# Kernel tuning notes

Hardware: AMD Instinct MI355X
Metric: run time of the kernel (lower is better)

Reference implementation:

```python
import jax, jax.numpy as jnp
import numpy as np

N_POINTS = 262144
SP_FEAT = 128
HIDDEN = 64
EMBED = 256
NUM_SP = 4096
NUM_SP2 = 256
PAD_LIMIT = 64
MASK_RATIO = 0.6


def setup_inputs() -> dict:
    key = jax.random.key(0)
    ks = jax.random.split(key, 6)
    x = jax.random.normal(ks[0], (N_POINTS, SP_FEAT), jnp.float32)
    # point -> superpoint ids, sorted; force every superpoint non-empty
    idx10 = jax.random.randint(ks[1], (N_POINTS,), 0, NUM_SP)
    idx10 = jnp.sort(idx10.at[:NUM_SP].set(jnp.arange(NUM_SP))).astype(jnp.int32)
    # superpoint -> higher superpoint, balanced (16 per group, < PAD_LIMIT), sorted
    idx21 = ((jnp.arange(NUM_SP) * NUM_SP2) // NUM_SP).astype(jnp.int32)
    # deterministic mask: exactly int(NUM_SP * MASK_RATIO) superpoints masked
    mask_num = int(NUM_SP * MASK_RATIO)
    perm = jax.random.permutation(ks[2], NUM_SP)
    is_masked = jnp.zeros((NUM_SP,), bool).at[perm[:mask_num]].set(True)
    W1 = jax.random.normal(ks[3], (SP_FEAT, HIDDEN), jnp.float32) / np.sqrt(SP_FEAT).astype(np.float32)
    b1 = jnp.zeros((HIDDEN,), jnp.float32)
    W2 = jax.random.normal(ks[4], (HIDDEN, EMBED), jnp.float32) / np.sqrt(HIDDEN).astype(np.float32)
    b2 = jnp.zeros((EMBED,), jnp.float32)
    return {
        "full_features": x,
        "full_super_indices_10": idx10,
        "full_super_indices_21": idx21,
        "is_masked": is_masked,
        "W1": W1, "b1": b1, "W2": W2, "b2": b2,
    }


def _pad_scatter(tokens, idx21, flag):
    # tokens: [NUM_SP, C]; idx21 sorted sp->sp2 ids; flag: [NUM_SP] bool.
    # rank of each flagged superpoint within its sp2 group (in sp order)
    f = flag.astype(jnp.int32)
    cum = jnp.cumsum(f)                                            # inclusive global cumsum
    per_group = jax.ops.segment_sum(f, idx21, num_segments=NUM_SP2)
    prefix = jnp.concatenate([jnp.zeros((1,), jnp.int32), jnp.cumsum(per_group)[:-1]])
    rank = cum - 1 - prefix[idx21]                                 # 0-based slot within group
    slot = jnp.where(flag, rank, PAD_LIMIT)                        # PAD_LIMIT -> dropped
    out = jnp.zeros((NUM_SP2, PAD_LIMIT, tokens.shape[-1]), tokens.dtype)
    return out.at[idx21, slot].set(tokens, mode="drop")


def reference(full_features, full_super_indices_10, full_super_indices_21,
              is_masked, W1, b1, W2, b2):
    # per-point 2-layer MLP (gather is implicit: MLP is pointwise), then segment max
    h = jax.nn.relu(full_features @ W1 + b1)                       # [N, HIDDEN]
    h = jax.nn.relu(h @ W2 + b2)                                   # [N, EMBED]
    tok = jax.ops.segment_max(h, full_super_indices_10, num_segments=NUM_SP)  # [NUM_SP, EMBED]
    remain_tokens = _pad_scatter(tok, full_super_indices_21, ~is_masked)      # [NUM_SP2, PAD, EMBED]
    mask_tokens = _pad_scatter(tok, full_super_indices_21, is_masked)         # [NUM_SP2, PAD, EMBED]
    return (remain_tokens, mask_tokens)
```

## Files before the change

### kernel.cpp

```cpp
#include <hip/hip_runtime.h>
#include <hip/hip_bf16.h>

#define N_POINTS 262144
#define SP_FEAT 128
#define HIDDEN 64
#define EMBED 256
#define NUM_SP 4096
#define NUM_SP2 256
#define PAD_LIMIT 64
#define SLOTS 4
#define OS_STRIDE 268

typedef __bf16 bf16x8 __attribute__((ext_vector_type(8)));
typedef float floatx4 __attribute__((ext_vector_type(4)));
using bf16 = __hip_bfloat16;

__global__ void prep_kernel(const float* __restrict__ W1, const float* __restrict__ W2,
                            const int* __restrict__ idx10,
                            bf16* __restrict__ W1t, bf16* __restrict__ W2t,
                            int* __restrict__ start) {
    int i = blockIdx.x * blockDim.x + threadIdx.x;
    if (i < HIDDEN * SP_FEAT) {
        int n = i >> 7, k = i & 127;
        W1t[i] = __float2bfloat16(W1[k * HIDDEN + n]);
    } else if (i < HIDDEN * SP_FEAT + EMBED * HIDDEN) {
        int j = i - HIDDEN * SP_FEAT;
        int n = j >> 6, k = j & 63;
        W2t[j] = __float2bfloat16(W2[k * EMBED + n]);
    } else if (i <= HIDDEN * SP_FEAT + EMBED * HIDDEN + NUM_SP) {
        int s = i - (HIDDEN * SP_FEAT + EMBED * HIDDEN);
        if (s == NUM_SP) { start[s] = N_POINTS; return; }
        int a = 0, b = N_POINTS;
        while (a < b) { int m = (a + b) >> 1; if (idx10[m] < s) a = m + 1; else b = m; }
        start[s] = a;
    }
}

__global__ __launch_bounds__(256) void rank_kernel(
    const int* __restrict__ idx21, const void* __restrict__ is_masked,
    int* __restrict__ invR, int* __restrict__ invM) {
    __shared__ int encS;
    const int tid = threadIdx.x;
    if (tid == 0) encS = 0;
    __syncthreads();
    const unsigned char* mb = (const unsigned char*)is_masked;
    const int* mi = (const int*)is_masked;
    int local = 0;
    for (int p = tid; p < NUM_SP; p += 256)
        if ((p & 3) && mb[p]) local = 1;
    if (local) atomicOr(&encS, 1);
    __syncthreads();
    const int e = encS;

    const int g = tid;
    int a = 0, b = NUM_SP;
    while (a < b) { int m = (a + b) >> 1; if (idx21[m] < g) a = m + 1; else b = m; }
    int lo = a;
    b = NUM_SP;
    while (a < b) { int m = (a + b) >> 1; if (idx21[m] < g + 1) a = m + 1; else b = m; }
    int hi = a;
    int nR = 0, nM = 0;
    for (int s = lo; s < hi; ++s) {
        int msk = e ? (int)mb[s] : mi[s];
        if (msk) { if (nM < PAD_LIMIT) invM[g * PAD_LIMIT + nM] = s; nM++; }
        else     { if (nR < PAD_LIMIT) invR[g * PAD_LIMIT + nR] = s; nR++; }
    }
    for (int r = nR; r < PAD_LIMIT; ++r) invR[g * PAD_LIMIT + r] = -1;
    for (int r = nM; r < PAD_LIMIT; ++r) invM[g * PAD_LIMIT + r] = -1;
}

__global__ __launch_bounds__(256) void mlp_segmax_kernel(
    const float* __restrict__ X, const int* __restrict__ idx10,
    const int* __restrict__ start,
    const bf16* __restrict__ W1t, const float* __restrict__ b1,
    const bf16* __restrict__ W2t, const float* __restrict__ b2,
    float* __restrict__ partial)
{
    __shared__ __align__(16) char smemU[64 * OS_STRIDE * 2];
    __shared__ __align__(16) bf16 H1s[64][72];
    __shared__ int sIdx[64];
    bf16 (*Xs)[136]      = (bf16(*)[136])smemU;
    bf16 (*Os)[OS_STRIDE] = (bf16(*)[OS_STRIDE])smemU;

    const int tid  = threadIdx.x;
    const int lane = tid & 63;
    const int w    = tid >> 6;
    const int l15  = lane & 15;
    const int quad = lane >> 4;
    const int b    = blockIdx.x;
    const int m0   = b * 64;

    bf16x8 bw1[4];
    {
        const bf16* p = W1t + (16 * w + l15) * SP_FEAT + quad * 8;
#pragma unroll
        for (int ks = 0; ks < 4; ++ks) bw1[ks] = *(const bf16x8*)(p + 32 * ks);
    }
    bf16x8 bf2[4][2];
#pragma unroll
    for (int tn = 0; tn < 4; ++tn) {
        const bf16* p = W2t + (64 * w + 16 * tn + l15) * HIDDEN + quad * 8;
#pragma unroll
        for (int ks = 0; ks < 2; ++ks) bf2[tn][ks] = *(const bf16x8*)(p + 32 * ks);
    }
    float b2f[4];
#pragma unroll
    for (int tn = 0; tn < 4; ++tn) b2f[tn] = b2[64 * w + 16 * tn + l15];
    const float b1v = b1[16 * w + l15];

#pragma unroll
    for (int i = 0; i < 4; ++i) {
        int c   = tid + 256 * i;
        int row = c >> 4;
        int cc  = (c & 15) * 8;
        const float* src = X + (size_t)(m0 + row) * SP_FEAT + cc;
        float4 u0 = *(const float4*)src;
        float4 u1 = *(const float4*)(src + 4);
        union { bf16x8 v; bf16 h[8]; } u;
        u.h[0] = __float2bfloat16(u0.x); u.h[1] = __float2bfloat16(u0.y);
        u.h[2] = __float2bfloat16(u0.z); u.h[3] = __float2bfloat16(u0.w);
        u.h[4] = __float2bfloat16(u1.x); u.h[5] = __float2bfloat16(u1.y);
        u.h[6] = __float2bfloat16(u1.z); u.h[7] = __float2bfloat16(u1.w);
        *(bf16x8*)(&Xs[row][cc]) = u.v;
    }
    if (tid < 64) sIdx[tid] = idx10[m0 + tid];
    __syncthreads();

    floatx4 zero4 = {0.f, 0.f, 0.f, 0.f};
    floatx4 acc1[4] = {zero4, zero4, zero4, zero4};
#pragma unroll
    for (int ks = 0; ks < 4; ++ks) {
        int k = ks * 32 + quad * 8;
#pragma unroll
        for (int tm = 0; tm < 4; ++tm) {
            bf16x8 a = *(bf16x8*)(&Xs[16 * tm + l15][k]);
            acc1[tm] = __builtin_amdgcn_mfma_f32_16x16x32_bf16(a, bw1[ks], acc1[tm], 0, 0, 0);
        }
    }
#pragma unroll
    for (int tm = 0; tm < 4; ++tm) {
#pragma unroll
        for (int r = 0; r < 4; ++r) {
            float v = acc1[tm][r] + b1v;
            v = v > 0.f ? v : 0.f;
            H1s[16 * tm + quad * 4 + r][16 * w + l15] = __float2bfloat16(v);
        }
    }
    __syncthreads();

#pragma unroll
    for (int tm = 0; tm < 4; ++tm) {
        bf16x8 a0 = *(bf16x8*)(&H1s[16 * tm + l15][quad * 8]);
        bf16x8 a1 = *(bf16x8*)(&H1s[16 * tm + l15][32 + quad * 8]);
#pragma unroll
        for (int tn = 0; tn < 4; ++tn) {
            floatx4 acc = zero4;
            acc = __builtin_amdgcn_mfma_f32_16x16x32_bf16(a0, bf2[tn][0], acc, 0, 0, 0);
            acc = __builtin_amdgcn_mfma_f32_16x16x32_bf16(a1, bf2[tn][1], acc, 0, 0, 0);
#pragma unroll
            for (int r = 0; r < 4; ++r) {
                float v = acc[r] + b2f[tn];
                v = v > 0.f ? v : 0.f;
                Os[16 * tm + quad * 4 + r][64 * w + 16 * tn + l15] = __float2bfloat16(v);
            }
        }
    }
    __syncthreads();

    {
        int cur_sp = sIdx[0];
        float cur  = __bfloat162float(Os[0][tid]);
        for (int r = 1; r < 64; ++r) {
            int sp = sIdx[r];
            float v = __bfloat162float(Os[r][tid]);
            if (sp != cur_sp) {
                int slot = b - (start[cur_sp] >> 6);
                int* dst = (int*)(partial + ((size_t)cur_sp * SLOTS + (slot < 3 ? slot : 3)) * EMBED + tid);
                if (slot < 3) *(float*)dst = cur;
                else atomicMax(dst, __float_as_int(cur));
                cur_sp = sp;
                cur = v;
            } else {
                cur = fmaxf(cur, v);
            }
        }
        int slot = b - (start[cur_sp] >> 6);
        int* dst = (int*)(partial + ((size_t)cur_sp * SLOTS + (slot < 3 ? slot : 3)) * EMBED + tid);
        if (slot < 3) *(float*)dst = cur;
        else atomicMax(dst, __float_as_int(cur));
    }
}

__global__ __launch_bounds__(256) void scatter_kernel(
    const float* __restrict__ partial, const int* __restrict__ invR,
    const int* __restrict__ invM, float* __restrict__ out)
{
    const int bb   = blockIdx.x;
    const int g    = bb & (NUM_SP2 - 1);
    const int slab = bb >> 8;
    const int tid  = threadIdx.x;
    const int* tab = slab ? invM : invR;
    float* o = out + ((size_t)slab * NUM_SP2 + g) * PAD_LIMIT * EMBED;
#pragma unroll 4
    for (int row = 0; row < PAD_LIMIT; ++row) {
        int sp = tab[g * PAD_LIMIT + row];
        float v = 0.f;
        if (sp >= 0) {
            const float* p = partial + (size_t)sp * SLOTS * EMBED + tid;
            v = fmaxf(fmaxf(p[0], p[EMBED]), fmaxf(p[2 * EMBED], p[3 * EMBED]));
        }
        o[row * EMBED + tid] = v;
    }
}

extern "C" void kernel_launch(void* const* d_in, const int* in_sizes, int n_in,
                              void* d_out, int out_size, void* d_ws, size_t ws_size,
                              hipStream_t stream) {
    (void)in_sizes; (void)n_in; (void)ws_size; (void)out_size;
    const float* X        = (const float*)d_in[0];
    const int* idx10      = (const int*)d_in[1];
    const int* idx21      = (const int*)d_in[2];
    const void* is_masked = (const void*)d_in[3];
    const float* W1       = (const float*)d_in[4];
    const float* b1       = (const float*)d_in[5];
    const float* W2       = (const float*)d_in[6];
    const float* b2       = (const float*)d_in[7];
    float* out            = (float*)d_out;

    char* ws      = (char*)d_ws;
    float* partial = (float*)ws;
    bf16* W1t     = (bf16*)(ws + (size_t)NUM_SP * SLOTS * EMBED * 4);
    bf16* W2t     = W1t + HIDDEN * SP_FEAT;
    int*  start   = (int*)((char*)(W2t + EMBED * HIDDEN));
    int*  invR    = start + (NUM_SP + 2);
    int*  invM    = invR + NUM_SP2 * PAD_LIMIT;

    hipMemsetAsync(partial, 0, (size_t)NUM_SP * SLOTS * EMBED * sizeof(float), stream);

    const int prep_n = HIDDEN * SP_FEAT + EMBED * HIDDEN + NUM_SP + 1;
    prep_kernel<<<(prep_n + 255) / 256, 256, 0, stream>>>(W1, W2, idx10, W1t, W2t, start);
    rank_kernel<<<1, 256, 0, stream>>>(idx21, is_masked, invR, invM);
    mlp_segmax_kernel<<<N_POINTS / 64, 256, 0, stream>>>(
        X, idx10, start, W1t, b1, W2t, b2, partial);
    scatter_kernel<<<NUM_SP2 * 2, 256, 0, stream>>>(partial, invR, invM, out);
}
```

Measured before the change: 272.5 us.

## Fuse memset, prep and rank kernels; alias H1 into shared buffer; vectorize scatter

Folds the memset of the partial buffer, the weight transpose/start search and the rank computation into one fused prep launch, removing two launches plus a memset. In the MLP kernel, H1 is aliased into the shared X/O buffer, padding strides change and launch bounds request four blocks per CU, which reduces LDS use to raise occupancy; an extra barrier is added so H1 fragments are loaded into registers before the output tile overwrites them. The scatter kernel now uses float4 loads and stores. These are several unrelated tweaks, and the extra register-held fragments may add pressure.

```diff
diff --git a/kernel.cpp b/kernel.cpp
--- a/kernel.cpp
+++ b/kernel.cpp
@@ -9,38 +9,52 @@
 #define NUM_SP2 256
 #define PAD_LIMIT 64
 #define SLOTS 4
-#define OS_STRIDE 268
+#define OS_STRIDE 260
+#define H1_STRIDE 76
 
 typedef __bf16 bf16x8 __attribute__((ext_vector_type(8)));
 typedef float floatx4 __attribute__((ext_vector_type(4)));
 using bf16 = __hip_bfloat16;
 
-__global__ void prep_kernel(const float* __restrict__ W1, const float* __restrict__ W2,
-                            const int* __restrict__ idx10,
-                            bf16* __restrict__ W1t, bf16* __restrict__ W2t,
-                            int* __restrict__ start) {
-    int i = blockIdx.x * blockDim.x + threadIdx.x;
-    if (i < HIDDEN * SP_FEAT) {
-        int n = i >> 7, k = i & 127;
-        W1t[i] = __float2bfloat16(W1[k * HIDDEN + n]);
-    } else if (i < HIDDEN * SP_FEAT + EMBED * HIDDEN) {
-        int j = i - HIDDEN * SP_FEAT;
-        int n = j >> 6, k = j & 63;
-        W2t[j] = __float2bfloat16(W2[k * EMBED + n]);
-    } else if (i <= HIDDEN * SP_FEAT + EMBED * HIDDEN + NUM_SP) {
-        int s = i - (HIDDEN * SP_FEAT + EMBED * HIDDEN);
-        if (s == NUM_SP) { start[s] = N_POINTS; return; }
-        int a = 0, b = N_POINTS;
-        while (a < b) { int m = (a + b) >> 1; if (idx10[m] < s) a = m + 1; else b = m; }
-        start[s] = a;
-    }
-}
-
-__global__ __launch_bounds__(256) void rank_kernel(
-    const int* __restrict__ idx21, const void* __restrict__ is_masked,
-    int* __restrict__ invR, int* __restrict__ invM) {
+__global__ __launch_bounds__(256) void fused_prep_kernel(
+    const float* __restrict__ W1, const float* __restrict__ W2,
+    const int* __restrict__ idx10, const int* __restrict__ idx21,
+    const void* __restrict__ is_masked,
+    bf16* __restrict__ W1t, bf16* __restrict__ W2t,
+    int* __restrict__ start, int* __restrict__ invR, int* __restrict__ invM,
+    float4* __restrict__ partial4)
+{
+    const int tid = threadIdx.x;
+    const int blk = blockIdx.x;
+
+    if (blk < 1024) {
+        int z = blk * 256 + tid;
+        float4 zv = {0.f, 0.f, 0.f, 0.f};
+#pragma unroll
+        for (int j = 0; j < 4; ++j)
+            partial4[z + j * (1024 * 256)] = zv;
+        return;
+    }
+    const int blk2 = blk - 1024;
+    if (blk2 < 113) {
+        int i = blk2 * 256 + tid;
+        if (i < HIDDEN * SP_FEAT) {
+            int n = i >> 7, k = i & 127;
+            W1t[i] = __float2bfloat16(W1[k * HIDDEN + n]);
+        } else if (i < HIDDEN * SP_FEAT + EMBED * HIDDEN) {
+            int j = i - HIDDEN * SP_FEAT;
+            int n = j >> 6, k = j & 63;
+            W2t[j] = __float2bfloat16(W2[k * EMBED + n]);
+        } else if (i <= HIDDEN * SP_FEAT + EMBED * HIDDEN + NUM_SP) {
+            int s = i - (HIDDEN * SP_FEAT + EMBED * HIDDEN);
+            if (s == NUM_SP) { start[s] = N_POINTS; return; }
+            int a = 0, b = N_POINTS;
+            while (a < b) { int m = (a + b) >> 1; if (idx10[m] < s) a = m + 1; else b = m; }
+            start[s] = a;
+        }
+        return;
+    }
     __shared__ int encS;
-    const int tid = threadIdx.x;
     if (tid == 0) encS = 0;
     __syncthreads();
     const unsigned char* mb = (const unsigned char*)is_masked;
@@ -69,7 +83,7 @@
     for (int r = nM; r < PAD_LIMIT; ++r) invM[g * PAD_LIMIT + r] = -1;
 }
 
-__global__ __launch_bounds__(256) void mlp_segmax_kernel(
+__global__ __launch_bounds__(256, 4) void mlp_segmax_kernel(
     const float* __restrict__ X, const int* __restrict__ idx10,
     const int* __restrict__ start,
     const bf16* __restrict__ W1t, const float* __restrict__ b1,
@@ -77,10 +91,10 @@
     float* __restrict__ partial)
 {
     __shared__ __align__(16) char smemU[64 * OS_STRIDE * 2];
-    __shared__ __align__(16) bf16 H1s[64][72];
     __shared__ int sIdx[64];
-    bf16 (*Xs)[136]      = (bf16(*)[136])smemU;
-    bf16 (*Os)[OS_STRIDE] = (bf16(*)[OS_STRIDE])smemU;
+    bf16 (*Xs)[136]       = (bf16(*)[136])smemU;
+    bf16 (*H1s)[H1_STRIDE] = (bf16(*)[H1_STRIDE])(smemU + 64 * 136 * 2);
+    bf16 (*Os)[OS_STRIDE]  = (bf16(*)[OS_STRIDE])smemU;
 
     const int tid  = threadIdx.x;
     const int lane = tid & 63;
@@ -148,15 +162,21 @@
     }
     __syncthreads();
 
+    bf16x8 afr[4][2];
 #pragma unroll
     for (int tm = 0; tm < 4; ++tm) {
-        bf16x8 a0 = *(bf16x8*)(&H1s[16 * tm + l15][quad * 8]);
-        bf16x8 a1 = *(bf16x8*)(&H1s[16 * tm + l15][32 + quad * 8]);
+        afr[tm][0] = *(bf16x8*)(&H1s[16 * tm + l15][quad * 8]);
+        afr[tm][1] = *(bf16x8*)(&H1s[16 * tm + l15][32 + quad * 8]);
+    }
+    __syncthreads();
+
+#pragma unroll
+    for (int tm = 0; tm < 4; ++tm) {
 #pragma unroll
         for (int tn = 0; tn < 4; ++tn) {
             floatx4 acc = zero4;
-            acc = __builtin_amdgcn_mfma_f32_16x16x32_bf16(a0, bf2[tn][0], acc, 0, 0, 0);
-            acc = __builtin_amdgcn_mfma_f32_16x16x32_bf16(a1, bf2[tn][1], acc, 0, 0, 0);
+            acc = __builtin_amdgcn_mfma_f32_16x16x32_bf16(afr[tm][0], bf2[tn][0], acc, 0, 0, 0);
+            acc = __builtin_amdgcn_mfma_f32_16x16x32_bf16(afr[tm][1], bf2[tn][1], acc, 0, 0, 0);
 #pragma unroll
             for (int r = 0; r < 4; ++r) {
                 float v = acc[r] + b2f[tn];
@@ -192,24 +212,31 @@
 }
 
 __global__ __launch_bounds__(256) void scatter_kernel(
-    const float* __restrict__ partial, const int* __restrict__ invR,
-    const int* __restrict__ invM, float* __restrict__ out)
+    const float4* __restrict__ partial4, const int* __restrict__ invR,
+    const int* __restrict__ invM, float4* __restrict__ out4)
 {
     const int bb   = blockIdx.x;
     const int g    = bb & (NUM_SP2 - 1);
     const int slab = bb >> 8;
     const int tid  = threadIdx.x;
+    const int c4   = tid & 63;
+    const int r0   = tid >> 6;
     const int* tab = slab ? invM : invR;
-    float* o = out + ((size_t)slab * NUM_SP2 + g) * PAD_LIMIT * EMBED;
+    float4* o = out4 + ((size_t)slab * NUM_SP2 + g) * PAD_LIMIT * 64;
 #pragma unroll 4
-    for (int row = 0; row < PAD_LIMIT; ++row) {
+    for (int rr = 0; rr < 16; ++rr) {
+        int row = r0 + rr * 4;
         int sp = tab[g * PAD_LIMIT + row];
-        float v = 0.f;
+        float4 v = {0.f, 0.f, 0.f, 0.f};
         if (sp >= 0) {
-            const float* p = partial + (size_t)sp * SLOTS * EMBED + tid;
-            v = fmaxf(fmaxf(p[0], p[EMBED]), fmaxf(p[2 * EMBED], p[3 * EMBED]));
-        }
-        o[row * EMBED + tid] = v;
+            const float4* p = partial4 + (size_t)sp * SLOTS * 64 + c4;
+            float4 a = p[0], bq = p[64], c = p[128], d = p[192];
+            v.x = fmaxf(fmaxf(a.x, bq.x), fmaxf(c.x, d.x));
+            v.y = fmaxf(fmaxf(a.y, bq.y), fmaxf(c.y, d.y));
+            v.z = fmaxf(fmaxf(a.z, bq.z), fmaxf(c.z, d.z));
+            v.w = fmaxf(fmaxf(a.w, bq.w), fmaxf(c.w, d.w));
+        }
+        o[row * 64 + c4] = v;
     }
 }
 
@@ -225,22 +252,20 @@
     const float* b1       = (const float*)d_in[5];
     const float* W2       = (const float*)d_in[6];
     const float* b2       = (const float*)d_in[7];
-    float* out            = (float*)d_out;
-
-    char* ws      = (char*)d_ws;
+
+    char* ws       = (char*)d_ws;
     float* partial = (float*)ws;
-    bf16* W1t     = (bf16*)(ws + (size_t)NUM_SP * SLOTS * EMBED * 4);
-    bf16* W2t     = W1t + HIDDEN * SP_FEAT;
-    int*  start   = (int*)((char*)(W2t + EMBED * HIDDEN));
-    int*  invR    = start + (NUM_SP + 2);
-    int*  invM    = invR + NUM_SP2 * PAD_LIMIT;
-
-    hipMemsetAsync(partial, 0, (size_t)NUM_SP * SLOTS * EMBED * sizeof(float), stream);
-
-    const int prep_n = HIDDEN * SP_FEAT + EMBED * HIDDEN + NUM_SP + 1;
-    prep_kernel<<<(prep_n + 255) / 256, 256, 0, stream>>>(W1, W2, idx10, W1t, W2t, start);
-    rank_kernel<<<1, 256, 0, stream>>>(idx21, is_masked, invR, invM);
+    bf16* W1t      = (bf16*)(ws + (size_t)NUM_SP * SLOTS * EMBED * 4);
+    bf16* W2t      = W1t + HIDDEN * SP_FEAT;
+    int*  start    = (int*)((char*)(W2t + EMBED * HIDDEN));
+    int*  invR     = start + (NUM_SP + 2);
+    int*  invM     = invR + NUM_SP2 * PAD_LIMIT;
+
+    fused_prep_kernel<<<1138, 256, 0, stream>>>(
+        W1, W2, idx10, idx21, is_masked, W1t, W2t, start, invR, invM,
+        (float4*)partial);
     mlp_segmax_kernel<<<N_POINTS / 64, 256, 0, stream>>>(
         X, idx10, start, W1t, b1, W2t, b2, partial);
-    scatter_kernel<<<NUM_SP2 * 2, 256, 0, stream>>>(partial, invR, invM, out);
-}
+    scatter_kernel<<<NUM_SP2 * 2, 256, 0, stream>>>(
+        (const float4*)partial, invR, invM, (float4*)d_out);
+}
```

New measurement: 263.1 us. -3.5%, faster.
